# Kernel tuning notes

Measured on AMD Instinct MI355X. Metric: run time of the kernel, lower is better.

## Reference

```python
import jax, jax.numpy as jnp
import numpy as np

N = 100000      # nodes
E = 1600000     # edges
G = 2048        # graphs
IN_DIM = 32
PEP_DIM = 768
H = 64          # hidden_dim
L = 3           # num_layers
BN_EPS = 1e-5


def setup_inputs() -> dict:
    key = jax.random.key(0)
    ks = jax.random.split(key, 32)
    x = jax.random.normal(ks[0], (N, IN_DIM), dtype=jnp.float32)
    edge_index = jax.random.randint(ks[1], (2, E), 0, N, dtype=jnp.int32)
    batch_idx = jnp.sort(jax.random.randint(ks[2], (N,), 0, G, dtype=jnp.int32))
    edge_attr = jax.random.normal(ks[3], (E, 2), dtype=jnp.float32)
    peptide_emb = jax.random.normal(ks[4], (G, PEP_DIM), dtype=jnp.float32)
    s = 0.1
    p = {
        'in_w': jax.random.normal(ks[5], (IN_DIM, H)) * s,
        'in_b': jnp.zeros((H,)),
        'e_w': jax.random.normal(ks[6], (2, H)) * s,
        'e_b': jnp.zeros((H,)),
        'conv_w1': jax.random.normal(ks[7], (L, H, H)) * s,
        'conv_b1': jnp.zeros((L, H)),
        'conv_w2': jax.random.normal(ks[8], (L, H, H)) * s,
        'conv_b2': jnp.zeros((L, H)),
        'bn_w': jnp.ones((L, H)),
        'bn_b': jnp.zeros((L, H)),
        'bn_mean': jnp.zeros((L, H)),
        'bn_var': jnp.ones((L, H)),
        'vn_w1': jax.random.normal(ks[9], (H, H)) * s,
        'vn_b1': jnp.zeros((H,)),
        'vn_w2': jax.random.normal(ks[10], (H, H)) * s,
        'vn_b2': jnp.zeros((H,)),
        'pep_w': jax.random.normal(ks[11], (PEP_DIM, H)) * s,
        'pep_b': jnp.zeros((H,)),
        'cls_w1': jax.random.normal(ks[12], (2 * H, H)) * s,
        'cls_b1': jnp.zeros((H,)),
        'cls_w2': jax.random.normal(ks[13], (H, 1)) * s,
        'cls_b2': jnp.zeros((1,)),
    }
    out = {'x': x, 'edge_index': edge_index, 'batch_idx': batch_idx,
           'edge_attr': edge_attr, 'peptide_emb': peptide_emb}
    out.update(p)
    return out


def reference(x, edge_index, batch_idx, edge_attr, peptide_emb,
              in_w, in_b, e_w, e_b,
              conv_w1, conv_b1, conv_w2, conv_b2,
              bn_w, bn_b, bn_mean, bn_var,
              vn_w1, vn_b1, vn_w2, vn_b2,
              pep_w, pep_b, cls_w1, cls_b1, cls_w2, cls_b2):
    seg = jax.ops.segment_sum
    src, dst = edge_index[0], edge_index[1]

    h = x @ in_w + in_b                       # [N,H]
    e = edge_attr @ e_w + e_b                 # [E,H]
    vn = jnp.zeros((G, H), dtype=h.dtype)     # virtual node per graph

    for i in range(L):
        h = h + vn[batch_idx]
        # GINE conv: (1+eps)*h + sum_j relu(h_j + e_ji), eps=0
        msg = jax.nn.relu(h[src] + e)                 # [E,H]
        agg = seg(msg, dst, num_segments=N)           # scatter-add to targets
        z = h + agg
        m = jax.nn.relu(z @ conv_w1[i] + conv_b1[i]) @ conv_w2[i] + conv_b2[i]
        # BatchNorm (eval: running stats)
        m = (m - bn_mean[i]) * jax.lax.rsqrt(bn_var[i] + BN_EPS) * bn_w[i] + bn_b[i]
        h = jax.nn.relu(m)                            # dropout = identity (eval)
        if i != L - 1:
            pooled = seg(h, batch_idx, num_segments=G)
            vn = vn + (jax.nn.relu(pooled @ vn_w1 + vn_b1) @ vn_w2 + vn_b2)

    # mean pooling
    counts = seg(jnp.ones((N,), dtype=h.dtype), batch_idx, num_segments=G)
    graph_emb = seg(h, batch_idx, num_segments=G) / jnp.maximum(counts, 1.0)[:, None]

    pep_hidden = jax.nn.relu(peptide_emb @ pep_w + pep_b)  # dropout = identity
    fused = jnp.concatenate([graph_emb, pep_hidden], axis=1)  # [G,2H]
    logits = (jax.nn.relu(fused @ cls_w1 + cls_b1) @ cls_w2 + cls_b2).reshape(-1)
    return logits
```

## Files before the change

### kernel.cpp

```cpp
#include <hip/hip_runtime.h>

#define NN 100000
#define NE 1600000
#define NG 2048
#define IN_DIM 32
#define PEP_DIM 768
#define H 64
#define BN_EPS 1e-5f
#define CONV_W 16
#define BUCK_SHIFT 9
#define NBUCK ((NN + 511) >> 9)
#define NBLKA 256
#define CHUNK ((NE + NBLKA - 1) / NBLKA)

typedef unsigned int uint;
typedef unsigned short ushort;
typedef __attribute__((ext_vector_type(8))) __bf16 bf16x8;
typedef __attribute__((ext_vector_type(4))) float f32x4;

__device__ __forceinline__ float bf2f(uint u) {
    return __uint_as_float((u & 0xFFFFu) << 16);
}
__device__ __forceinline__ uint f2bf(float x) {
    uint b = __float_as_uint(x);
    return (b + 0x7FFFu + ((b >> 16) & 1u)) >> 16;
}


__global__ __launch_bounds__(256) void k_hist(const int* __restrict__ ei, int* __restrict__ mat) {
    __shared__ int hloc[NBUCK];
    for (int i = threadIdx.x; i < NBUCK; i += 256) hloc[i] = 0;
    __syncthreads();
    int base = blockIdx.x * CHUNK;
    int end = min(NE, base + CHUNK);
    for (int e = base + threadIdx.x; e < end; e += 256)
        atomicAdd(&hloc[ei[NE + e] >> BUCK_SHIFT], 1);
    __syncthreads();
    for (int i = threadIdx.x; i < NBUCK; i += 256)
        mat[i * NBLKA + blockIdx.x] = hloc[i];
}

__global__ __launch_bounds__(NBLKA) void k_s1(int* __restrict__ mat, int* __restrict__ tot) {
    __shared__ int s[NBLKA];
    int b = blockIdx.x;
    int v = mat[b * NBLKA + threadIdx.x];
    s[threadIdx.x] = v;
    __syncthreads();
    for (int off = 1; off < NBLKA; off <<= 1) {
        int x = (threadIdx.x >= off) ? s[threadIdx.x - off] : 0;
        __syncthreads();
        s[threadIdx.x] += x;
        __syncthreads();
    }
    mat[b * NBLKA + threadIdx.x] = s[threadIdx.x] - v;
    if (threadIdx.x == NBLKA - 1) tot[b] = s[threadIdx.x];
}

__global__ __launch_bounds__(256) void k_s2(const int* __restrict__ tot, int* __restrict__ bases) {
    __shared__ int s[256];
    int v = (threadIdx.x < NBUCK) ? tot[threadIdx.x] : 0;
    s[threadIdx.x] = v;
    __syncthreads();
    for (int off = 1; off < 256; off <<= 1) {
        int x = (threadIdx.x >= off) ? s[threadIdx.x - off] : 0;
        __syncthreads();
        s[threadIdx.x] += x;
        __syncthreads();
    }
    if (threadIdx.x < NBUCK) bases[threadIdx.x] = s[threadIdx.x] - v;
    if (threadIdx.x == 255) bases[NBUCK] = s[255];
}

__global__ __launch_bounds__(256) void k_scat1(const int* __restrict__ ei, const float* __restrict__ ea,
                                               const int* __restrict__ mat, const int* __restrict__ bases,
                                               int2* __restrict__ tmp) {
    __shared__ int cur[NBUCK];
    for (int i = threadIdx.x; i < NBUCK; i += 256)
        cur[i] = bases[i] + mat[i * NBLKA + blockIdx.x];
    __syncthreads();
    int base = blockIdx.x * CHUNK;
    int end = min(NE, base + CHUNK);
    for (int e = base + threadIdx.x; e < end; e += 256) {
        int dst = ei[NE + e];
        int bk = dst >> BUCK_SHIFT;
        int pos = atomicAdd(&cur[bk], 1);
        float2 a = *(const float2*)(ea + (size_t)e * 2);
        int2 r;
        r.x = ei[e] | ((dst & 511) << 17);
        r.y = (int)(f2bf(a.x) | (f2bf(a.y) << 16));
        tmp[pos] = r;
    }
}

__global__ __launch_bounds__(256) void k_scat2(const int2* __restrict__ tmp, const int* __restrict__ bases,
                                               int2* __restrict__ csr, int* __restrict__ row_start) {
    __shared__ int deg[512];
    __shared__ int psc[256];
    __shared__ int cur[512];
    int b = blockIdx.x;
    int t = threadIdx.x;
    int s0 = bases[b], s1 = bases[b + 1];
    deg[2 * t] = 0; deg[2 * t + 1] = 0;
    __syncthreads();
    for (int e = s0 + t; e < s1; e += 256)
        atomicAdd(&deg[(tmp[e].x >> 17) & 511], 1);
    __syncthreads();
    int d0 = deg[2 * t], d1 = deg[2 * t + 1];
    psc[t] = d0 + d1;
    __syncthreads();
    for (int off = 1; off < 256; off <<= 1) {
        int x = (t >= off) ? psc[t - off] : 0;
        __syncthreads();
        psc[t] += x;
        __syncthreads();
    }
    int ep = psc[t] - (d0 + d1);
    int node0 = (b << BUCK_SHIFT) + 2 * t;
    int e0 = s0 + ep, e1 = e0 + d0;
    cur[2 * t] = e0; cur[2 * t + 1] = e1;
    if (node0 < NN) row_start[node0] = e0;
    if (node0 + 1 < NN) row_start[node0 + 1] = e1;
    __syncthreads();
    for (int e = s0 + t; e < s1; e += 256) {
        int2 r = tmp[e];
        int nl = (r.x >> 17) & 511;
        int pos = atomicAdd(&cur[nl], 1);
        int2 o;
        o.x = r.x & 0x1FFFF;
        o.y = r.y;
        csr[pos] = o;
    }
    if (b == NBUCK - 1 && t == 0) row_start[NN] = NE;
}

__global__ void k_gstart(const int* __restrict__ batch, int* __restrict__ gstart) {
    int i = blockIdx.x * 256 + threadIdx.x;
    if (i >= NN) return;
    int b = batch[i];
    int p = (i == 0) ? -1 : batch[i - 1];
    for (int g = p + 1; g <= b; g++) gstart[g] = i;
    if (i == NN - 1) {
        for (int g = b + 1; g <= NG; g++) gstart[g] = NN;
    }
}

__global__ void k_init_h(const float* __restrict__ x, const float* __restrict__ w,
                         const float* __restrict__ b, ushort* __restrict__ h) {
    int t = blockIdx.x * 256 + threadIdx.x;
    int node = t >> 4;
    if (node >= NN) return;
    int c4 = (t & 15) * 4;
    float4 acc = *(const float4*)(b + c4);
    const float* xr = x + node * IN_DIM;
    for (int k = 0; k < IN_DIM; k++) {
        float xv = xr[k];
        float4 wv = *(const float4*)(w + k * H + c4);
        acc.x += xv * wv.x; acc.y += xv * wv.y;
        acc.z += xv * wv.z; acc.w += xv * wv.w;
    }
    uint2 o;
    o.x = f2bf(acc.x) | (f2bf(acc.y) << 16);
    o.y = f2bf(acc.z) | (f2bf(acc.w) << 16);
    *(uint2*)(h + (size_t)node * H + c4) = o;
}

__global__ void k_prep(const float* __restrict__ w1, const float* __restrict__ w2,
                       ushort* __restrict__ wp) {
    int t = blockIdx.x * 256 + threadIdx.x;
    if (t >= 3 * 8192) return;
    int j = t & 7;
    int lane = (t >> 3) & 63;
    int ct = (t >> 9) & 3;
    int ks = (t >> 11) & 1;
    int st = (t >> 12) & 1;
    int ly = t >> 13;
    int k = ks * 32 + (lane >> 4) * 8 + j;
    int c = ct * 16 + (lane & 15);
    const float* src = (st == 0) ? w1 : w2;
    wp[t] = (ushort)f2bf(src[ly * H * H + k * H + c]);
}

__global__ __launch_bounds__(1024, 4) void k_gather(
    const ushort* __restrict__ h_in, ushort* __restrict__ z,
    const int2* __restrict__ csr, const int* __restrict__ row_start,
    const float* __restrict__ ew, const float* __restrict__ eb) {
    int w = threadIdx.x >> 6;
    int c = threadIdx.x & 63;
    int node = blockIdx.x * CONV_W + w;
    float ew0 = ew[c], ew1 = ew[H + c], ebc = eb[c];
    int rs = __builtin_amdgcn_readfirstlane(row_start[node]);
    int re = __builtin_amdgcn_readfirstlane(row_start[node + 1]);
    float acc = 0.f;
    int j = rs;
    for (; j + 16 <= re; j += 16) {
        int2 v[16];
        #pragma unroll
        for (int t = 0; t < 16; t++) v[t] = csr[j + t];
        float hh[16];
        #pragma unroll
        for (int t = 0; t < 16; t++) hh[t] = bf2f(h_in[(size_t)v[t].x * H + c]);
        #pragma unroll
        for (int t = 0; t < 16; t++)
            acc += fmaxf(hh[t] + fmaf(bf2f(v[t].y), ew0, fmaf(bf2f((uint)v[t].y >> 16), ew1, ebc)), 0.f);
    }
    for (; j + 4 <= re; j += 4) {
        int2 v[4];
        #pragma unroll
        for (int t = 0; t < 4; t++) v[t] = csr[j + t];
        float hh[4];
        #pragma unroll
        for (int t = 0; t < 4; t++) hh[t] = bf2f(h_in[(size_t)v[t].x * H + c]);
        #pragma unroll
        for (int t = 0; t < 4; t++)
            acc += fmaxf(hh[t] + fmaf(bf2f(v[t].y), ew0, fmaf(bf2f((uint)v[t].y >> 16), ew1, ebc)), 0.f);
    }
    for (; j < re; j++) {
        int2 v = csr[j];
        float hs = bf2f(h_in[(size_t)v.x * H + c]);
        acc += fmaxf(hs + fmaf(bf2f(v.y), ew0, fmaf(bf2f((uint)v.y >> 16), ew1, ebc)), 0.f);
    }
    float zv = bf2f(h_in[(size_t)node * H + c]) + acc;
    uint me = f2bf(zv);
    uint nb2 = __shfl_down(me, 1, 64);
    if ((c & 1) == 0) {
        *(uint*)(z + (size_t)node * H + c) = me | (nb2 << 16);
    }
}

__global__ __launch_bounds__(256, 4) void k_mlp(
    const ushort* __restrict__ z, ushort* __restrict__ h_out,
    const ushort* __restrict__ wp,
    const float* __restrict__ b1, const float* __restrict__ b2,
    const float* __restrict__ bnw, const float* __restrict__ bnb,
    const float* __restrict__ bnm, const float* __restrict__ bnv) {
    __shared__ ushort ts[4][16][72];
    int w = threadIdx.x >> 6;
    int l = threadIdx.x & 63;
    int nb = blockIdx.x * 64 + w * 16;
    if (nb >= NN) return;
    int r = l & 15;
    int kg = l >> 4;
    const ushort* zr = z + (size_t)(nb + r) * H + kg * 8;
    bf16x8 A0 = *(const bf16x8*)(zr);
    bf16x8 A1 = *(const bf16x8*)(zr + 32);
    f32x4 acc[4];
    #pragma unroll
    for (int ct = 0; ct < 4; ct++) {
        bf16x8 B0 = *(const bf16x8*)(wp + (0 * 4 + ct) * 512 + l * 8);
        bf16x8 B1 = *(const bf16x8*)(wp + (1 * 4 + ct) * 512 + l * 8);
        f32x4 a = {0.f, 0.f, 0.f, 0.f};
        a = __builtin_amdgcn_mfma_f32_16x16x32_bf16(A0, B0, a, 0, 0, 0);
        a = __builtin_amdgcn_mfma_f32_16x16x32_bf16(A1, B1, a, 0, 0, 0);
        acc[ct] = a;
    }
    #pragma unroll
    for (int ct = 0; ct < 4; ct++) {
        int col = ct * 16 + r;
        float bb = b1[col];
        #pragma unroll
        for (int q = 0; q < 4; q++) {
            float tv = fmaxf(acc[ct][q] + bb, 0.f);
            ts[w][kg * 4 + q][col] = (ushort)f2bf(tv);
        }
    }
    bf16x8 T0 = *(const bf16x8*)(&ts[w][r][kg * 8]);
    bf16x8 T1 = *(const bf16x8*)(&ts[w][r][32 + kg * 8]);
    f32x4 acc2[4];
    #pragma unroll
    for (int ct = 0; ct < 4; ct++) {
        bf16x8 B0 = *(const bf16x8*)(wp + 4096 + (0 * 4 + ct) * 512 + l * 8);
        bf16x8 B1 = *(const bf16x8*)(wp + 4096 + (1 * 4 + ct) * 512 + l * 8);
        f32x4 a = {0.f, 0.f, 0.f, 0.f};
        a = __builtin_amdgcn_mfma_f32_16x16x32_bf16(T0, B0, a, 0, 0, 0);
        a = __builtin_amdgcn_mfma_f32_16x16x32_bf16(T1, B1, a, 0, 0, 0);
        acc2[ct] = a;
    }
    #pragma unroll
    for (int ct = 0; ct < 4; ct++) {
        int col = ct * 16 + r;
        float bb2 = b2[col];
        float mean = bnm[col];
        float sc = bnw[col] * rsqrtf(bnv[col] + BN_EPS);
        float bo = bnb[col];
        #pragma unroll
        for (int q = 0; q < 4; q++) {
            float hv = fmaxf((acc2[ct][q] + bb2 - mean) * sc + bo, 0.f);
            ts[w][kg * 4 + q][col] = (ushort)f2bf(hv);
        }
    }
    #pragma unroll
    for (int it = 0; it < 4; it++) {
        int flat = it * 64 + l;
        int node = flat >> 4;
        int ch4 = (flat & 15) * 4;
        uint2 val = *(uint2*)(&ts[w][node][ch4]);
        *(uint2*)(h_out + (size_t)(nb + node) * H + ch4) = val;
    }
}

__global__ __launch_bounds__(256) void k_poolvn(ushort* __restrict__ h,
                                                const int* __restrict__ gstart,
                                                float* __restrict__ pooled,
                                                const float* __restrict__ w1, const float* __restrict__ b1,
                                                const float* __restrict__ w2, const float* __restrict__ b2,
                                                float* __restrict__ vn, int do_vn) {
    __shared__ float ps[4][H];
    __shared__ float ts[4][H];
    int w = threadIdx.x >> 6, c = threadIdx.x & 63;
    int g = blockIdx.x * 4 + w;
    int s = __builtin_amdgcn_readfirstlane(gstart[g]);
    int e = __builtin_amdgcn_readfirstlane(gstart[g + 1]);
    float acc = 0.f;
    int n = s;
    for (; n + 4 <= e; n += 4) {
        float x0 = bf2f(h[(size_t)(n + 0) * H + c]);
        float x1 = bf2f(h[(size_t)(n + 1) * H + c]);
        float x2 = bf2f(h[(size_t)(n + 2) * H + c]);
        float x3 = bf2f(h[(size_t)(n + 3) * H + c]);
        acc += x0; acc += x1; acc += x2; acc += x3;
    }
    for (; n < e; n++) acc += bf2f(h[(size_t)n * H + c]);
    pooled[(size_t)g * H + c] = acc;
    if (!do_vn) return;
    ps[w][c] = acc;
    float a1 = b1[c];
    for (int k = 0; k < H; k += 4) {
        float4 pv = *(const float4*)&ps[w][k];
        a1 = fmaf(pv.x, w1[(k + 0) * H + c], a1);
        a1 = fmaf(pv.y, w1[(k + 1) * H + c], a1);
        a1 = fmaf(pv.z, w1[(k + 2) * H + c], a1);
        a1 = fmaf(pv.w, w1[(k + 3) * H + c], a1);
    }
    ts[w][c] = fmaxf(a1, 0.f);
    float a2 = b2[c];
    for (int k = 0; k < H; k += 4) {
        float4 tv = *(const float4*)&ts[w][k];
        a2 = fmaf(tv.x, w2[(k + 0) * H + c], a2);
        a2 = fmaf(tv.y, w2[(k + 1) * H + c], a2);
        a2 = fmaf(tv.z, w2[(k + 2) * H + c], a2);
        a2 = fmaf(tv.w, w2[(k + 3) * H + c], a2);
    }
    float vnew = vn[(size_t)g * H + c] + a2;
    vn[(size_t)g * H + c] = vnew;
    ps[w][c] = vnew;
    float vlo = ps[w][(c & 31) * 2 + 0];
    float vhi = ps[w][(c & 31) * 2 + 1];
    int ch2 = (c & 31) * 2;
    for (n = s; n + 2 <= e; n += 2) {
        size_t off = (size_t)(n + (c >> 5)) * H + ch2;
        uint u = *(uint*)(h + off);
        float lo = bf2f(u) + vlo;
        float hi = bf2f(u >> 16) + vhi;
        *(uint*)(h + off) = f2bf(lo) | (f2bf(hi) << 16);
    }
    if (n < e && c < 32) {
        size_t off = (size_t)n * H + ch2;
        uint u = *(uint*)(h + off);
        float lo = bf2f(u) + vlo;
        float hi = bf2f(u >> 16) + vhi;
        *(uint*)(h + off) = f2bf(lo) | (f2bf(hi) << 16);
    }
}

__global__ __launch_bounds__(256) void k_final(const float* __restrict__ pooled,
                                               const int* __restrict__ gstart,
                                               const float* __restrict__ pep,
                                               const float* __restrict__ pw, const float* __restrict__ pb,
                                               const float* __restrict__ cw1, const float* __restrict__ cb1,
                                               const float* __restrict__ cw2, const float* __restrict__ cb2,
                                               float* __restrict__ out) {
    __shared__ float red[4][H];
    __shared__ float fused[2 * H];
    int g = blockIdx.x;
    int lane = threadIdx.x & 63;
    int part = threadIdx.x >> 6;
    const float* pr = pep + (size_t)g * PEP_DIM;
    float acc = 0.0f;
    int k0 = part * (PEP_DIM / 4);
    for (int k = k0; k < k0 + PEP_DIM / 4; k++) {
        acc += pr[k] * pw[k * H + lane];
    }
    red[part][lane] = acc;
    __syncthreads();
    if (part == 0) {
        float s = red[0][lane] + red[1][lane] + red[2][lane] + red[3][lane] + pb[lane];
        fused[H + lane] = fmaxf(s, 0.0f);
        float c = (float)(gstart[g + 1] - gstart[g]);
        float invc = 1.0f / fmaxf(c, 1.0f);
        fused[lane] = pooled[(size_t)g * H + lane] * invc;
    }
    __syncthreads();
    if (part == 0) {
        float a = cb1[lane];
        for (int k = 0; k < 2 * H; k++) a += fused[k] * cw1[k * H + lane];
        float t = fmaxf(a, 0.0f);
        float v = t * cw2[lane];
        for (int off = 32; off > 0; off >>= 1) v += __shfl_down(v, off, 64);
        if (lane == 0) out[g] = v + cb2[0];
    }
}

extern "C" void kernel_launch(void* const* d_in, const int* in_sizes, int n_in,
                              void* d_out, int out_size, void* d_ws, size_t ws_size,
                              hipStream_t stream) {
    const float* x        = (const float*)d_in[0];
    const int*   ei       = (const int*)d_in[1];
    const int*   batch    = (const int*)d_in[2];
    const float* ea       = (const float*)d_in[3];
    const float* pep      = (const float*)d_in[4];
    const float* in_w     = (const float*)d_in[5];
    const float* in_b     = (const float*)d_in[6];
    const float* e_w      = (const float*)d_in[7];
    const float* e_b      = (const float*)d_in[8];
    const float* conv_w1  = (const float*)d_in[9];
    const float* conv_b1  = (const float*)d_in[10];
    const float* conv_w2  = (const float*)d_in[11];
    const float* conv_b2  = (const float*)d_in[12];
    const float* bn_w     = (const float*)d_in[13];
    const float* bn_b     = (const float*)d_in[14];
    const float* bn_mean  = (const float*)d_in[15];
    const float* bn_var   = (const float*)d_in[16];
    const float* vn_w1    = (const float*)d_in[17];
    const float* vn_b1    = (const float*)d_in[18];
    const float* vn_w2    = (const float*)d_in[19];
    const float* vn_b2    = (const float*)d_in[20];
    const float* pep_w    = (const float*)d_in[21];
    const float* pep_b    = (const float*)d_in[22];
    const float* cls_w1   = (const float*)d_in[23];
    const float* cls_b1   = (const float*)d_in[24];
    const float* cls_w2   = (const float*)d_in[25];
    const float* cls_b2   = (const float*)d_in[26];
    float* out = (float*)d_out;

    ushort* h_a   = (ushort*)d_ws;
    ushort* h_b   = h_a + (size_t)NN * H;
    ushort* z     = h_b + (size_t)NN * H;
    int2*  tmp    = (int2*)z;
    float* pooled = (float*)(z + (size_t)NN * H);
    float* vn     = pooled + (size_t)NG * H;
    int2*  csr    = (int2*)(vn + (size_t)NG * H);
    ushort* wp    = (ushort*)(csr + (size_t)NE);
    int* row_start = (int*)(wp + 3 * 8192);
    int* gstart    = row_start + NN + 16;
    int* mat       = gstart + NG + 16;
    int* tot       = mat + NBUCK * NBLKA;
    int* bases     = tot + NBUCK;

    k_hist<<<NBLKA, 256, 0, stream>>>(ei, mat);
    k_s1<<<NBUCK, NBLKA, 0, stream>>>(mat, tot);
    k_s2<<<1, 256, 0, stream>>>(tot, bases);
    k_scat1<<<NBLKA, 256, 0, stream>>>(ei, ea, mat, bases, tmp);
    k_scat2<<<NBUCK, 256, 0, stream>>>(tmp, bases, csr, row_start);
    k_gstart<<<(NN + 255) / 256, 256, 0, stream>>>(batch, gstart);
    k_prep<<<(3 * 8192 + 255) / 256, 256, 0, stream>>>(conv_w1, conv_w2, wp);

    k_init_h<<<NN * 16 / 256, 256, 0, stream>>>(x, in_w, in_b, h_a);
    hipMemsetAsync(vn, 0, (size_t)NG * H * sizeof(float), stream);

    ushort* hc = h_a;
    ushort* hn = h_b;
    for (int i = 0; i < 3; i++) {
        k_gather<<<NN / CONV_W, 1024, 0, stream>>>(hc, z, csr, row_start, e_w, e_b);
        k_mlp<<<(NN + 63) / 64, 256, 0, stream>>>(z, hn, wp + i * 8192,
                                                  conv_b1 + i * H, conv_b2 + i * H,
                                                  bn_w + i * H, bn_b + i * H,
                                                  bn_mean + i * H, bn_var + i * H);
        ushort* t = hc; hc = hn; hn = t;
        k_poolvn<<<NG / 4, 256, 0, stream>>>(hc, gstart, pooled,
                                             vn_w1, vn_b1, vn_w2, vn_b2, vn,
                                             (i < 2) ? 1 : 0);
    }

    k_final<<<NG, 256, 0, stream>>>(pooled, gstart, pep, pep_w, pep_b,
                                    cls_w1, cls_b1, cls_w2, cls_b2, out);
}
```

Baseline: 349.6 us.

## Fuse neighbor gather and MLP into one per-layer kernel via LDS tiles

Merges the gather kernel and the MFMA MLP kernel into a single k_layer kernel. Each wave now aggregates 16 consecutive nodes one after another, stages the bf16 z rows in shared memory, and then runs the two-layer MLP with BatchNorm directly from LDS. This removes the global write and re-read of the z buffer and one kernel launch per layer. In exchange, far fewer waves are launched and each one walks its 16 nodes serially, which lowers memory-level parallelism on the latency-bound gather and can leave a tail of imbalanced waves.

```diff
diff --git a/kernel.cpp b/kernel.cpp
--- a/kernel.cpp
+++ b/kernel.cpp
@@ -7,7 +7,8 @@
 #define PEP_DIM 768
 #define H 64
 #define BN_EPS 1e-5f
-#define CONV_W 16
+#define NT16 (NN / 16)
+#define LAYER_BLOCKS 512
 #define BUCK_SHIFT 9
 #define NBUCK ((NN + 511) >> 9)
 #define NBLKA 256
@@ -180,70 +181,62 @@
     wp[t] = (ushort)f2bf(src[ly * H * H + k * H + c]);
 }
 
-__global__ __launch_bounds__(1024, 4) void k_gather(
-    const ushort* __restrict__ h_in, ushort* __restrict__ z,
+__global__ __launch_bounds__(1024, 4) void k_layer(
+    const ushort* __restrict__ h_in, ushort* __restrict__ h_out,
     const int2* __restrict__ csr, const int* __restrict__ row_start,
-    const float* __restrict__ ew, const float* __restrict__ eb) {
-    int w = threadIdx.x >> 6;
-    int c = threadIdx.x & 63;
-    int node = blockIdx.x * CONV_W + w;
-    float ew0 = ew[c], ew1 = ew[H + c], ebc = eb[c];
-    int rs = __builtin_amdgcn_readfirstlane(row_start[node]);
-    int re = __builtin_amdgcn_readfirstlane(row_start[node + 1]);
-    float acc = 0.f;
-    int j = rs;
-    for (; j + 16 <= re; j += 16) {
-        int2 v[16];
-        #pragma unroll
-        for (int t = 0; t < 16; t++) v[t] = csr[j + t];
-        float hh[16];
-        #pragma unroll
-        for (int t = 0; t < 16; t++) hh[t] = bf2f(h_in[(size_t)v[t].x * H + c]);
-        #pragma unroll
-        for (int t = 0; t < 16; t++)
-            acc += fmaxf(hh[t] + fmaf(bf2f(v[t].y), ew0, fmaf(bf2f((uint)v[t].y >> 16), ew1, ebc)), 0.f);
-    }
-    for (; j + 4 <= re; j += 4) {
-        int2 v[4];
-        #pragma unroll
-        for (int t = 0; t < 4; t++) v[t] = csr[j + t];
-        float hh[4];
-        #pragma unroll
-        for (int t = 0; t < 4; t++) hh[t] = bf2f(h_in[(size_t)v[t].x * H + c]);
-        #pragma unroll
-        for (int t = 0; t < 4; t++)
-            acc += fmaxf(hh[t] + fmaf(bf2f(v[t].y), ew0, fmaf(bf2f((uint)v[t].y >> 16), ew1, ebc)), 0.f);
-    }
-    for (; j < re; j++) {
-        int2 v = csr[j];
-        float hs = bf2f(h_in[(size_t)v.x * H + c]);
-        acc += fmaxf(hs + fmaf(bf2f(v.y), ew0, fmaf(bf2f((uint)v.y >> 16), ew1, ebc)), 0.f);
-    }
-    float zv = bf2f(h_in[(size_t)node * H + c]) + acc;
-    uint me = f2bf(zv);
-    uint nb2 = __shfl_down(me, 1, 64);
-    if ((c & 1) == 0) {
-        *(uint*)(z + (size_t)node * H + c) = me | (nb2 << 16);
-    }
-}
-
-__global__ __launch_bounds__(256, 4) void k_mlp(
-    const ushort* __restrict__ z, ushort* __restrict__ h_out,
+    const float* __restrict__ ew, const float* __restrict__ eb,
     const ushort* __restrict__ wp,
     const float* __restrict__ b1, const float* __restrict__ b2,
     const float* __restrict__ bnw, const float* __restrict__ bnb,
     const float* __restrict__ bnm, const float* __restrict__ bnv) {
-    __shared__ ushort ts[4][16][72];
+    __shared__ ushort zs[16][16][72];
     int w = threadIdx.x >> 6;
     int l = threadIdx.x & 63;
-    int nb = blockIdx.x * 64 + w * 16;
-    if (nb >= NN) return;
+    int tile = w * LAYER_BLOCKS + blockIdx.x;
+    if (tile >= NT16) return;
+    int nb = tile * 16;
+    float ew0 = ew[l], ew1 = ew[H + l], ebc = eb[l];
+    for (int g = 0; g < 16; g++) {
+        int node = nb + g;
+        int rs = __builtin_amdgcn_readfirstlane(row_start[node]);
+        int re = __builtin_amdgcn_readfirstlane(row_start[node + 1]);
+        float acc = 0.f;
+        int j = rs;
+        for (; j + 16 <= re; j += 16) {
+            int2 v[16];
+            #pragma unroll
+            for (int t = 0; t < 16; t++) v[t] = csr[j + t];
+            float hh[16];
+            #pragma unroll
+            for (int t = 0; t < 16; t++) hh[t] = bf2f(h_in[(size_t)v[t].x * H + l]);
+            #pragma unroll
+            for (int t = 0; t < 16; t++)
+                acc += fmaxf(hh[t] + fmaf(bf2f(v[t].y), ew0, fmaf(bf2f((uint)v[t].y >> 16), ew1, ebc)), 0.f);
+        }
+        for (; j + 4 <= re; j += 4) {
+            int2 v[4];
+            #pragma unroll
+            for (int t = 0; t < 4; t++) v[t] = csr[j + t];
+            float hh[4];
+            #pragma unroll
+            for (int t = 0; t < 4; t++) hh[t] = bf2f(h_in[(size_t)v[t].x * H + l]);
+            #pragma unroll
+            for (int t = 0; t < 4; t++)
+                acc += fmaxf(hh[t] + fmaf(bf2f(v[t].y), ew0, fmaf(bf2f((uint)v[t].y >> 16), ew1, ebc)), 0.f);
+        }
+        for (; j < re; j++) {
+            int2 v = csr[j];
+            float hs = bf2f(h_in[(size_t)v.x * H + l]);
+            acc += fmaxf(hs + fmaf(bf2f(v.y), ew0, fmaf(bf2f((uint)v.y >> 16), ew1, ebc)), 0.f);
+        }
+        float zv = bf2f(h_in[(size_t)node * H + l]) + acc;
+        zs[w][g][l] = (ushort)f2bf(zv);
+    }
     int r = l & 15;
     int kg = l >> 4;
-    const ushort* zr = z + (size_t)(nb + r) * H + kg * 8;
-    bf16x8 A0 = *(const bf16x8*)(zr);
-    bf16x8 A1 = *(const bf16x8*)(zr + 32);
-    f32x4 acc[4];
+    bf16x8 A0 = *(const bf16x8*)(&zs[w][r][kg * 8]);
+    bf16x8 A1 = *(const bf16x8*)(&zs[w][r][32 + kg * 8]);
+    f32x4 acc1[4];
     #pragma unroll
     for (int ct = 0; ct < 4; ct++) {
         bf16x8 B0 = *(const bf16x8*)(wp + (0 * 4 + ct) * 512 + l * 8);
@@ -251,7 +244,7 @@
         f32x4 a = {0.f, 0.f, 0.f, 0.f};
         a = __builtin_amdgcn_mfma_f32_16x16x32_bf16(A0, B0, a, 0, 0, 0);
         a = __builtin_amdgcn_mfma_f32_16x16x32_bf16(A1, B1, a, 0, 0, 0);
-        acc[ct] = a;
+        acc1[ct] = a;
     }
     #pragma unroll
     for (int ct = 0; ct < 4; ct++) {
@@ -259,12 +252,12 @@
         float bb = b1[col];
         #pragma unroll
         for (int q = 0; q < 4; q++) {
-            float tv = fmaxf(acc[ct][q] + bb, 0.f);
-            ts[w][kg * 4 + q][col] = (ushort)f2bf(tv);
+            float tv = fmaxf(acc1[ct][q] + bb, 0.f);
+            zs[w][kg * 4 + q][col] = (ushort)f2bf(tv);
         }
     }
-    bf16x8 T0 = *(const bf16x8*)(&ts[w][r][kg * 8]);
-    bf16x8 T1 = *(const bf16x8*)(&ts[w][r][32 + kg * 8]);
+    bf16x8 T0 = *(const bf16x8*)(&zs[w][r][kg * 8]);
+    bf16x8 T1 = *(const bf16x8*)(&zs[w][r][32 + kg * 8]);
     f32x4 acc2[4];
     #pragma unroll
     for (int ct = 0; ct < 4; ct++) {
@@ -285,7 +278,7 @@
         #pragma unroll
         for (int q = 0; q < 4; q++) {
             float hv = fmaxf((acc2[ct][q] + bb2 - mean) * sc + bo, 0.f);
-            ts[w][kg * 4 + q][col] = (ushort)f2bf(hv);
+            zs[w][kg * 4 + q][col] = (ushort)f2bf(hv);
         }
     }
     #pragma unroll
@@ -293,7 +286,7 @@
         int flat = it * 64 + l;
         int node = flat >> 4;
         int ch4 = (flat & 15) * 4;
-        uint2 val = *(uint2*)(&ts[w][node][ch4]);
+        uint2 val = *(uint2*)(&zs[w][node][ch4]);
         *(uint2*)(h_out + (size_t)(nb + node) * H + ch4) = val;
     }
 }
@@ -460,11 +453,11 @@
     ushort* hc = h_a;
     ushort* hn = h_b;
     for (int i = 0; i < 3; i++) {
-        k_gather<<<NN / CONV_W, 1024, 0, stream>>>(hc, z, csr, row_start, e_w, e_b);
-        k_mlp<<<(NN + 63) / 64, 256, 0, stream>>>(z, hn, wp + i * 8192,
-                                                  conv_b1 + i * H, conv_b2 + i * H,
-                                                  bn_w + i * H, bn_b + i * H,
-                                                  bn_mean + i * H, bn_var + i * H);
+        k_layer<<<LAYER_BLOCKS, 1024, 0, stream>>>(hc, hn, csr, row_start,
+                                                   e_w, e_b, wp + i * 8192,
+                                                   conv_b1 + i * H, conv_b2 + i * H,
+                                                   bn_w + i * H, bn_b + i * H,
+                                                   bn_mean + i * H, bn_var + i * H);
         ushort* t = hc; hc = hn; hn = t;
         k_poolvn<<<NG / 4, 256, 0, stream>>>(hc, gstart, pooled,
                                              vn_w1, vn_b1, vn_w2, vn_b2, vn,
```

After: 416.5 us. 1.19x slower.
